# Kernel tuning notes

Hardware: AMD Instinct MI355X
Metric: run time of the kernel (lower is better)

Reference implementation:

```python
import jax, jax.numpy as jnp
import numpy as np

WIN = 9
PAD = WIN // 2
LOSS_WEIGHT = 1.0


def _box_sum(x):
    # x: [B,1,H,W]; 9x9 box-filter sum via conv2d with a ones kernel (SAME padding)
    k = jnp.ones((1, 1, WIN, WIN), dtype=x.dtype)
    return jax.lax.conv_general_dilated(
        x, k, window_strides=(1, 1), padding=[(PAD, PAD), (PAD, PAD)],
        dimension_numbers=('NCHW', 'OIHW', 'NCHW'))


def _ncc_map(I, J):
    I2, J2, IJ = I * I, J * J, I * J
    I_sum = _box_sum(I)
    J_sum = _box_sum(J)
    I2_sum = _box_sum(I2)
    J2_sum = _box_sum(J2)
    IJ_sum = _box_sum(IJ)
    n = float(WIN * WIN)
    u_I = I_sum / n
    u_J = J_sum / n
    cross = IJ_sum - u_J * I_sum - u_I * J_sum + u_I * u_J * n
    I_var = I2_sum - 2.0 * u_I * I_sum + u_I * u_I * n
    J_var = J2_sum - 2.0 * u_J * J_sum + u_J * u_J * n
    cc = cross * cross / (I_var * J_var + 1e-5)
    return 1.0 - cc


def setup_inputs() -> dict:
    key = jax.random.key(0)
    k1, k2, k3 = jax.random.split(key, 3)
    shape = (32, 1, 512, 512)
    return {
        'img1': jax.random.uniform(k1, shape, dtype=jnp.float32),
        'img2': jax.random.uniform(k2, shape, dtype=jnp.float32),
        'fusion_img': jax.random.uniform(k3, shape, dtype=jnp.float32),
    }


def reference(img1, img2, fusion_img):
    combined = (_ncc_map(img1, fusion_img) + _ncc_map(img2, fusion_img)) / 2.0
    return jnp.mean(combined) * LOSS_WEIGHT
```

## Files before the change

kernel.cpp:

```cpp
#include <hip/hip_runtime.h>

#define BATCH 32
#define H 512
#define W 512
#define PADR 4
#define WIN 9
#define SEG 16
#define COLS 8
#define NT 64
#define NSTEP (SEG + WIN - 1)
#define SCALE (0.5f / 8388608.0f)

typedef float v4f __attribute__((ext_vector_type(4)));


__device__ __forceinline__ float from_left(float v) {
    return __builtin_bit_cast(float, __builtin_amdgcn_update_dpp(
        0, __builtin_bit_cast(int, v), 0x138, 0xF, 0xF, true));
}
__device__ __forceinline__ float from_right(float v) {
    return __builtin_bit_cast(float, __builtin_amdgcn_update_dpp(
        0, __builtin_bit_cast(int, v), 0x130, 0xF, 0xF, true));
}

#define EMITQ(qi) do {                                        \
    const float p1 = V[qi][0];                                \
    const float p2 = p1 + V[qi][1];                           \
    const float p3 = p2 + V[qi][2];                           \
    const float p4 = p3 + V[qi][3];                           \
    const float p5 = p4 + V[qi][4];                           \
    const float p6 = p5 + V[qi][5];                           \
    const float p7 = p6 + V[qi][6];                           \
    const float T  = p7 + V[qi][7];                           \
    const float l0 = from_left(T - p4);                       \
    const float l1 = from_left(T - p5);                       \
    const float l2 = from_left(T - p6);                       \
    const float l3 = from_left(V[qi][7]);         \
    const float r4 = from_right(p1);                          \
    const float r5 = from_right(p2);                          \
    const float r6 = from_right(p3);                          \
    const float r7 = from_right(p4);                          \
    S[qi][0] = l0 + p5;                                       \
    S[qi][1] = l1 + p6;                                       \
    S[qi][2] = l2 + p7;                                       \
    S[qi][3] = l3 + T;                                        \
    S[qi][4] = T + r4;                                        \
    S[qi][5] = (T - p1) + r5;                                 \
    S[qi][6] = (T - p2) + r6;                                 \
    S[qi][7] = (T - p3) + r7;                                 \
} while (0)

__global__ __launch_bounds__(NT, 1) void ncc_loss_kernel(
    const float* __restrict__ g1, const float* __restrict__ g2,
    const float* __restrict__ gf, float* __restrict__ out)
{
    const int t  = threadIdx.x;
    const int x0 = t * COLS;
    const int y0 = blockIdx.y * SEG;
    const int b  = blockIdx.z;
    const size_t base = (size_t)b * (size_t)(H * W);
    const int voff = x0 * 4;

    v4f buf[2][3][2];
    auto load_row = [&](int step, int par) {
        const int yr  = y0 - PADR + step;
        const int rec = ((unsigned)yr < (unsigned)H) ? (W * 4) : 0;
        const int yc  = yr < 0 ? 0 : (yr >= H ? H - 1 : yr);
        const size_t roff = base + (size_t)yc * W;
        __amdgpu_buffer_rsrc_t r1 = __builtin_amdgcn_make_buffer_rsrc(
            (void*)(g1 + roff), (short)0, rec, 0x00020000);
        __amdgpu_buffer_rsrc_t r2 = __builtin_amdgcn_make_buffer_rsrc(
            (void*)(g2 + roff), (short)0, rec, 0x00020000);
        __amdgpu_buffer_rsrc_t rf = __builtin_amdgcn_make_buffer_rsrc(
            (void*)(gf + roff), (short)0, rec, 0x00020000);
        buf[par][0][0] = __builtin_bit_cast(v4f,
            __builtin_amdgcn_raw_buffer_load_b128(r1, voff, 0, 0));
        buf[par][0][1] = __builtin_bit_cast(v4f,
            __builtin_amdgcn_raw_buffer_load_b128(r1, voff + 16, 0, 0));
        buf[par][1][0] = __builtin_bit_cast(v4f,
            __builtin_amdgcn_raw_buffer_load_b128(r2, voff, 0, 0));
        buf[par][1][1] = __builtin_bit_cast(v4f,
            __builtin_amdgcn_raw_buffer_load_b128(r2, voff + 16, 0, 0));
        buf[par][2][0] = __builtin_bit_cast(v4f,
            __builtin_amdgcn_raw_buffer_load_b128(rf, voff, 0, 0));
        buf[par][2][1] = __builtin_bit_cast(v4f,
            __builtin_amdgcn_raw_buffer_load_b128(rf, voff + 16, 0, 0));
    };

    float ring[3][WIN][COLS];
#pragma unroll
    for (int im = 0; im < 3; ++im)
#pragma unroll
        for (int i = 0; i < WIN; ++i)
#pragma unroll
            for (int c = 0; c < COLS; ++c) ring[im][i][c] = 0.f;

    float V[8][COLS];
#pragma unroll
    for (int q = 0; q < 8; ++q)
#pragma unroll
        for (int c = 0; c < COLS; ++c) V[q][c] = 0.f;

    float lsum = 0.f;
    const float inv_n = 1.0f / 81.0f;

    load_row(0, 0);

#pragma unroll
    for (int s = 0; s < NSTEP; ++s) {
        if (s + 1 < NSTEP) load_row(s + 1, (s + 1) & 1);

        const int ph = s % WIN;

#pragma unroll
        for (int c = 0; c < COLS; ++c) {
            const float n1 = buf[s & 1][0][c >> 2][c & 3];
            const float n2 = buf[s & 1][1][c >> 2][c & 3];
            const float nf = buf[s & 1][2][c >> 2][c & 3];
            const float o1 = ring[0][ph][c], o2 = ring[1][ph][c],
                        of = ring[2][ph][c];
            V[0][c] += n1 - o1;
            V[1][c] += n2 - o2;
            V[2][c] += nf - of;
            V[3][c] = fmaf(n1, n1, fmaf(-o1, o1, V[3][c]));
            V[4][c] = fmaf(n2, n2, fmaf(-o2, o2, V[4][c]));
            V[5][c] = fmaf(nf, nf, fmaf(-of, of, V[5][c]));
            V[6][c] = fmaf(n1, nf, fmaf(-o1, of, V[6][c]));
            V[7][c] = fmaf(n2, nf, fmaf(-o2, of, V[7][c]));
            ring[0][ph][c] = n1; ring[1][ph][c] = n2; ring[2][ph][c] = nf;
        }

        if (s >= WIN - 1) {
            float S[8][COLS];
            EMITQ(0); EMITQ(1); EMITQ(2); EMITQ(3);
            EMITQ(4); EMITQ(5); EMITQ(6); EMITQ(7);

#pragma unroll
            for (int c = 0; c < COLS; ++c) {
                const float sA = S[0][c], sC = S[1][c], sF = S[2][c];
                const float u1 = sA * inv_n;
                const float u2 = sC * inv_n;
                const float uf = sF * inv_n;
                const float cross1 = fmaf(-sA, uf, S[6][c]);
                const float var1   = fmaf(-sA, u1, S[3][c]);
                const float varf   = fmaf(-sF, uf, S[5][c]);
                const float cross2 = fmaf(-sC, uf, S[7][c]);
                const float var2   = fmaf(-sC, u2, S[4][c]);
                const float d1 = fmaf(var1, varf, 1e-5f);
                const float d2 = fmaf(var2, varf, 1e-5f);
                const float inv = __builtin_amdgcn_rcpf(d1 * d2);
                float num = cross1 * cross1 * d2;
                num = fmaf(cross2 * cross2, d1, num);
                lsum += fmaf(-num, inv, 2.0f);
            }
        }
    }

#pragma unroll
    for (int offd = 32; offd > 0; offd >>= 1)
        lsum += __shfl_down(lsum, offd);
    if (t == 0) atomicAdd(out, lsum * SCALE);
}

extern "C" void kernel_launch(void* const* d_in, const int* in_sizes, int n_in,
                              void* d_out, int out_size, void* d_ws, size_t ws_size,
                              hipStream_t stream) {
    const float* img1 = (const float*)d_in[0];
    const float* img2 = (const float*)d_in[1];
    const float* fimg = (const float*)d_in[2];
    float* out = (float*)d_out;

    hipMemsetAsync(out, 0, sizeof(float), stream);

    dim3 grid(1, H / SEG, BATCH);
    ncc_loss_kernel<<<grid, dim3(NT), 0, stream>>>(img1, img2, fimg, out);
}
```

Baseline: 134.6 us.

## Replace register ring buffer with reloaded outgoing rows and split epilogue halves

Removes the 9-row register ring (216 floats per thread) and instead reloads the row leaving the vertical window from global memory (likely cache-resident) into a small buffer. The horizontal emit/epilogue is split into low and high halves so only a 4-column S tile stays live at once, with tree-style prefix sums. This sharply cuts register pressure and static indexing work, at the cost of doubling global/L2 load traffic per step and adding load latency for the outgoing row.

```diff
diff --git a/kernel.cpp b/kernel.cpp
--- a/kernel.cpp
+++ b/kernel.cpp
@@ -23,11 +23,8 @@
         0, __builtin_bit_cast(int, v), 0x130, 0xF, 0xF, true));
 }
 
-#define EMITQ(qi) do {                                        \
-    const float p1 = V[qi][0];                                \
-    const float p2 = p1 + V[qi][1];                           \
-    const float p3 = p2 + V[qi][2];                           \
-    const float p4 = p3 + V[qi][3];                           \
+#define EMITQ_LO(qi) do {                                     \
+    const float p4 = (V[qi][0] + V[qi][1]) + (V[qi][2] + V[qi][3]); \
     const float p5 = p4 + V[qi][4];                           \
     const float p6 = p5 + V[qi][5];                           \
     const float p7 = p6 + V[qi][6];                           \
@@ -36,18 +33,47 @@
     const float l1 = from_left(T - p5);                       \
     const float l2 = from_left(T - p6);                       \
     const float l3 = from_left(V[qi][7]);         \
+    S[qi][0] = l0 + p5;                                       \
+    S[qi][1] = l1 + p6;                                       \
+    S[qi][2] = l2 + p7;                                       \
+    S[qi][3] = l3 + T;                                        \
+} while (0)
+
+#define EMITQ_HI(qi) do {                                     \
+    const float p1 = V[qi][0];                                \
+    const float p2 = p1 + V[qi][1];                           \
+    const float p3 = p2 + V[qi][2];                           \
+    const float p4 = p3 + V[qi][3];                           \
+    const float T  = p4 + ((V[qi][4] + V[qi][5]) + (V[qi][6] + V[qi][7])); \
     const float r4 = from_right(p1);                          \
     const float r5 = from_right(p2);                          \
     const float r6 = from_right(p3);                          \
     const float r7 = from_right(p4);                          \
-    S[qi][0] = l0 + p5;                                       \
-    S[qi][1] = l1 + p6;                                       \
-    S[qi][2] = l2 + p7;                                       \
-    S[qi][3] = l3 + T;                                        \
-    S[qi][4] = T + r4;                                        \
-    S[qi][5] = (T - p1) + r5;                                 \
-    S[qi][6] = (T - p2) + r6;                                 \
-    S[qi][7] = (T - p3) + r7;                                 \
+    S[qi][0] = T + r4;                                        \
+    S[qi][1] = (T - p1) + r5;                                 \
+    S[qi][2] = (T - p2) + r6;                                 \
+    S[qi][3] = (T - p3) + r7;                                 \
+} while (0)
+
+#define EPILOG4() do {                                        \
+    _Pragma("unroll")                                         \
+    for (int c = 0; c < 4; ++c) {                             \
+        const float sA = S[0][c], sC = S[1][c], sF = S[2][c]; \
+        const float u1 = sA * inv_n;                          \
+        const float u2 = sC * inv_n;                          \
+        const float uf = sF * inv_n;                          \
+        const float cross1 = fmaf(-sA, uf, S[6][c]);          \
+        const float var1   = fmaf(-sA, u1, S[3][c]);          \
+        const float varf   = fmaf(-sF, uf, S[5][c]);          \
+        const float cross2 = fmaf(-sC, uf, S[7][c]);          \
+        const float var2   = fmaf(-sC, u2, S[4][c]);          \
+        const float d1 = fmaf(var1, varf, 1e-5f);             \
+        const float d2 = fmaf(var2, varf, 1e-5f);             \
+        const float inv = __builtin_amdgcn_rcpf(d1 * d2);     \
+        float num = cross1 * cross1 * d2;                     \
+        num = fmaf(cross2 * cross2, d1, num);                 \
+        lsum += fmaf(-num, inv, 2.0f);                        \
+    }                                                         \
 } while (0)
 
 __global__ __launch_bounds__(NT, 1) void ncc_loss_kernel(
@@ -61,9 +87,10 @@
     const size_t base = (size_t)b * (size_t)(H * W);
     const int voff = x0 * 4;
 
-    v4f buf[2][3][2];
-    auto load_row = [&](int step, int par) {
-        const int yr  = y0 - PADR + step;
+    v4f nbuf[2][3][2];
+    v4f obuf[3][2];
+
+    auto issue6 = [&](int yr, v4f (*dst)[2]) {
         const int rec = ((unsigned)yr < (unsigned)H) ? (W * 4) : 0;
         const int yc  = yr < 0 ? 0 : (yr >= H ? H - 1 : yr);
         const size_t roff = base + (size_t)yc * W;
@@ -73,27 +100,19 @@
             (void*)(g2 + roff), (short)0, rec, 0x00020000);
         __amdgpu_buffer_rsrc_t rf = __builtin_amdgcn_make_buffer_rsrc(
             (void*)(gf + roff), (short)0, rec, 0x00020000);
-        buf[par][0][0] = __builtin_bit_cast(v4f,
+        dst[0][0] = __builtin_bit_cast(v4f,
             __builtin_amdgcn_raw_buffer_load_b128(r1, voff, 0, 0));
-        buf[par][0][1] = __builtin_bit_cast(v4f,
+        dst[0][1] = __builtin_bit_cast(v4f,
             __builtin_amdgcn_raw_buffer_load_b128(r1, voff + 16, 0, 0));
-        buf[par][1][0] = __builtin_bit_cast(v4f,
+        dst[1][0] = __builtin_bit_cast(v4f,
             __builtin_amdgcn_raw_buffer_load_b128(r2, voff, 0, 0));
-        buf[par][1][1] = __builtin_bit_cast(v4f,
+        dst[1][1] = __builtin_bit_cast(v4f,
             __builtin_amdgcn_raw_buffer_load_b128(r2, voff + 16, 0, 0));
-        buf[par][2][0] = __builtin_bit_cast(v4f,
+        dst[2][0] = __builtin_bit_cast(v4f,
             __builtin_amdgcn_raw_buffer_load_b128(rf, voff, 0, 0));
-        buf[par][2][1] = __builtin_bit_cast(v4f,
+        dst[2][1] = __builtin_bit_cast(v4f,
             __builtin_amdgcn_raw_buffer_load_b128(rf, voff + 16, 0, 0));
     };
-
-    float ring[3][WIN][COLS];
-#pragma unroll
-    for (int im = 0; im < 3; ++im)
-#pragma unroll
-        for (int i = 0; i < WIN; ++i)
-#pragma unroll
-            for (int c = 0; c < COLS; ++c) ring[im][i][c] = 0.f;
 
     float V[8][COLS];
 #pragma unroll
@@ -104,55 +123,52 @@
     float lsum = 0.f;
     const float inv_n = 1.0f / 81.0f;
 
-    load_row(0, 0);
+    issue6(y0 - PADR, nbuf[0]);
 
 #pragma unroll
     for (int s = 0; s < NSTEP; ++s) {
-        if (s + 1 < NSTEP) load_row(s + 1, (s + 1) & 1);
-
-        const int ph = s % WIN;
+        if (s + 1 < NSTEP) issue6(y0 - PADR + (s + 1), nbuf[(s + 1) & 1]);
 
 #pragma unroll
         for (int c = 0; c < COLS; ++c) {
-            const float n1 = buf[s & 1][0][c >> 2][c & 3];
-            const float n2 = buf[s & 1][1][c >> 2][c & 3];
-            const float nf = buf[s & 1][2][c >> 2][c & 3];
-            const float o1 = ring[0][ph][c], o2 = ring[1][ph][c],
-                        of = ring[2][ph][c];
-            V[0][c] += n1 - o1;
-            V[1][c] += n2 - o2;
-            V[2][c] += nf - of;
-            V[3][c] = fmaf(n1, n1, fmaf(-o1, o1, V[3][c]));
-            V[4][c] = fmaf(n2, n2, fmaf(-o2, o2, V[4][c]));
-            V[5][c] = fmaf(nf, nf, fmaf(-of, of, V[5][c]));
-            V[6][c] = fmaf(n1, nf, fmaf(-o1, of, V[6][c]));
-            V[7][c] = fmaf(n2, nf, fmaf(-o2, of, V[7][c]));
-            ring[0][ph][c] = n1; ring[1][ph][c] = n2; ring[2][ph][c] = nf;
+            const float n1 = nbuf[s & 1][0][c >> 2][c & 3];
+            const float n2 = nbuf[s & 1][1][c >> 2][c & 3];
+            const float nf = nbuf[s & 1][2][c >> 2][c & 3];
+            if (s >= WIN) {
+                const float o1 = obuf[0][c >> 2][c & 3];
+                const float o2 = obuf[1][c >> 2][c & 3];
+                const float of = obuf[2][c >> 2][c & 3];
+                V[0][c] += n1 - o1;
+                V[1][c] += n2 - o2;
+                V[2][c] += nf - of;
+                V[3][c] = fmaf(n1, n1, fmaf(-o1, o1, V[3][c]));
+                V[4][c] = fmaf(n2, n2, fmaf(-o2, o2, V[4][c]));
+                V[5][c] = fmaf(nf, nf, fmaf(-of, of, V[5][c]));
+                V[6][c] = fmaf(n1, nf, fmaf(-o1, of, V[6][c]));
+                V[7][c] = fmaf(n2, nf, fmaf(-o2, of, V[7][c]));
+            } else {
+                V[0][c] += n1;
+                V[1][c] += n2;
+                V[2][c] += nf;
+                V[3][c] = fmaf(n1, n1, V[3][c]);
+                V[4][c] = fmaf(n2, n2, V[4][c]);
+                V[5][c] = fmaf(nf, nf, V[5][c]);
+                V[6][c] = fmaf(n1, nf, V[6][c]);
+                V[7][c] = fmaf(n2, nf, V[7][c]);
+            }
         }
 
+        if (s + 1 >= WIN && s + 1 < NSTEP)
+            issue6(y0 - PADR + (s + 1) - WIN, obuf);
+
         if (s >= WIN - 1) {
-            float S[8][COLS];
-            EMITQ(0); EMITQ(1); EMITQ(2); EMITQ(3);
-            EMITQ(4); EMITQ(5); EMITQ(6); EMITQ(7);
-
-#pragma unroll
-            for (int c = 0; c < COLS; ++c) {
-                const float sA = S[0][c], sC = S[1][c], sF = S[2][c];
-                const float u1 = sA * inv_n;
-                const float u2 = sC * inv_n;
-                const float uf = sF * inv_n;
-                const float cross1 = fmaf(-sA, uf, S[6][c]);
-                const float var1   = fmaf(-sA, u1, S[3][c]);
-                const float varf   = fmaf(-sF, uf, S[5][c]);
-                const float cross2 = fmaf(-sC, uf, S[7][c]);
-                const float var2   = fmaf(-sC, u2, S[4][c]);
-                const float d1 = fmaf(var1, varf, 1e-5f);
-                const float d2 = fmaf(var2, varf, 1e-5f);
-                const float inv = __builtin_amdgcn_rcpf(d1 * d2);
-                float num = cross1 * cross1 * d2;
-                num = fmaf(cross2 * cross2, d1, num);
-                lsum += fmaf(-num, inv, 2.0f);
-            }
+            float S[8][4];
+            EMITQ_LO(0); EMITQ_LO(1); EMITQ_LO(2); EMITQ_LO(3);
+            EMITQ_LO(4); EMITQ_LO(5); EMITQ_LO(6); EMITQ_LO(7);
+            EPILOG4();
+            EMITQ_HI(0); EMITQ_HI(1); EMITQ_HI(2); EMITQ_HI(3);
+            EMITQ_HI(4); EMITQ_HI(5); EMITQ_HI(6); EMITQ_HI(7);
+            EPILOG4();
         }
     }
 
```

After: 136.5 us. About the same (+1.4%).
